# Performance work log

Measured on AMD Instinct MI355X. Metric: run time of the kernel, lower is better.

## Reference

```python
import jax, jax.numpy as jnp
import numpy as np

B, S, TLEN, IN_DI, H = 256, 512, 32, 5, 256  # batch, enc seq len, decode horizon, features, hidden


def setup_inputs() -> dict:
    key = jax.random.key(0)
    ks = jax.random.split(key, 20)
    sc = 0.06  # ~ 1/sqrt(H), matches torch LSTM/Linear uniform init scale
    def p(k, shape):
        return jax.random.normal(k, shape, jnp.float32) * sc
    return {
        "srcs": jax.random.normal(ks[0], (B, S, IN_DI), jnp.float32),
        # encoder LSTM layer 1 (in_di -> H), layer 2 (H -> H); b = b_ih + b_hh combined
        "wih_e1": p(ks[1], (4 * H, IN_DI)), "whh_e1": p(ks[2], (4 * H, H)), "b_e1": p(ks[3], (4 * H,)),
        "wih_e2": p(ks[4], (4 * H, H)), "whh_e2": p(ks[5], (4 * H, H)), "b_e2": p(ks[6], (4 * H,)),
        # decoder input projection Linear(in_di -> H)
        "wdi": p(ks[7], (H, IN_DI)), "bdi": p(ks[8], (H,)),
        # decoder LSTM layer 1 (H -> H), layer 2 (H -> H)
        "wih_d1": p(ks[9], (4 * H, H)), "whh_d1": p(ks[10], (4 * H, H)), "b_d1": p(ks[11], (4 * H,)),
        "wih_d2": p(ks[12], (4 * H, H)), "whh_d2": p(ks[13], (4 * H, H)), "b_d2": p(ks[14], (4 * H,)),
        # w: Linear(2H -> in_di); out_projection: Linear(in_di -> in_di)
        "ww": p(ks[15], (IN_DI, 2 * H)), "bw": p(ks[16], (IN_DI,)),
        "wop": p(ks[17], (IN_DI, IN_DI)), "bop": p(ks[18], (IN_DI,)),
    }


def _cell(h, c, gates_x, whh):
    # pytorch LSTM gate order: i, f, g, o
    g = gates_x + h @ whh.T
    i, f, gg, o = jnp.split(g, 4, axis=-1)
    c = jax.nn.sigmoid(f) * c + jax.nn.sigmoid(i) * jnp.tanh(gg)
    h = jax.nn.sigmoid(o) * jnp.tanh(c)
    return h, c


def _lstm(x, h0, c0, wih, whh, b):
    # x: [B, T, D] -> outs [B, T, H], final (h, c)
    xs = x @ wih.T + b  # precompute input projections [B, T, 4H]
    def step(carry, xt):
        h, c = _cell(carry[0], carry[1], xt, whh)
        return (h, c), h
    (h, c), ys = jax.lax.scan(step, (h0, c0), jnp.swapaxes(xs, 0, 1))
    return jnp.swapaxes(ys, 0, 1), h, c


def reference(srcs, wih_e1, whh_e1, b_e1, wih_e2, whh_e2, b_e2,
              wdi, bdi, wih_d1, whh_d1, b_d1, wih_d2, whh_d2, b_d2,
              ww, bw, wop, bop):
    Bv = srcs.shape[0]
    z = jnp.zeros((Bv, H), srcs.dtype)
    # encoder: two stacked LSTMs, zero initial state (dropout is identity in eval)
    e1, _, _ = _lstm(srcs, z, z, wih_e1, whh_e1, b_e1)
    enc_outs, h_enc, c_enc = _lstm(e1, z, z, wih_e2, whh_e2, b_e2)  # [B, S, H]

    def dec_step(carry, _):
        h, c, inp = carry
        x = inp @ wdi.T + bdi                               # dec_input projection [B, H]
        # decoder LSTM layer 1 seeded with carried hidden (source passes layer-2 hidden back in)
        h1, c1 = _cell(h, c, x @ wih_d1.T + b_d1, whh_d1)
        # decoder LSTM layer 2 re-zeroed every step (faithful to LSTMS_Decoder)
        h2, c2 = _cell(z, z, h1 @ wih_d2.T + b_d2, whh_d2)  # dec_out [B, H]
        energies = jnp.einsum('bh,bsh->bs', h2, enc_outs)   # dot attention
        weights = jax.nn.softmax(energies, axis=0)          # softmax over dim=0 (batch!), as in source
        context = jnp.einsum('bs,bsh->bh', weights, enc_outs)
        cats = jnp.concatenate([h2, context], axis=-1) @ ww.T + bw
        pred = jnp.tanh(cats) @ wop.T + bop                 # [B, in_di]
        return (h2, c2, pred), (pred, context)

    inp0 = jnp.ones((Bv, IN_DI), srcs.dtype)
    _, (preds, ctxs) = jax.lax.scan(dec_step, (h_enc, c_enc, inp0), None, length=TLEN)
    out = jnp.swapaxes(preds, 0, 1)        # [B, tlen, in_di]
    context_enc = jnp.swapaxes(ctxs, 0, 1)  # [B, tlen, H]
    return out, context_enc
```

## Files before the change

### kernel.cpp

```cpp
#include <hip/hip_runtime.h>
#include <hip/hip_bf16.h>

#define B_    256
#define S_    512
#define H_    256
#define TLEN_ 32
#define DI_   5
#define ENCSTRIDE 131072
#define CHUNK 32
#define NCHUNK 16
#define NB 2

__device__ __forceinline__ float bf2f(unsigned short v) {
    return __uint_as_float(((unsigned)v) << 16);
}
__device__ __forceinline__ unsigned short f2bf(float f) {
    __hip_bfloat16 h = __float2bfloat16(f);
    return *reinterpret_cast<unsigned short*>(&h);
}

__global__ __launch_bounds__(256) void init_kernel(float* PRD) {
    int i = blockIdx.x * 256 + threadIdx.x;
    if (i < B_ * DI_) PRD[i] = 1.0f;
}

__global__ __launch_bounds__(256) void packbf_kernel(const float* __restrict__ m,
                                                     ushort4* __restrict__ out) {
    int idx = blockIdx.x * 256 + threadIdx.x;
    int k4 = idx >> 10, n = idx & 1023;
    float4 v = ((const float4*)m)[n * 64 + k4];
    out[idx] = make_ushort4(f2bf(v.x), f2bf(v.y), f2bf(v.z), f2bf(v.w));
}

__global__ __launch_bounds__(256) void weff_kernel(const float* __restrict__ wih_d1,
                                                   const float* __restrict__ wdi,
                                                   const float* __restrict__ bdi,
                                                   const float* __restrict__ b_d1,
                                                   float* __restrict__ weff,
                                                   float* __restrict__ beff) {
    int n = blockIdx.x * 256 + threadIdx.x;
    float acc[DI_] = {0.f, 0.f, 0.f, 0.f, 0.f};
    float accb = 0.f;
    for (int k = 0; k < H_; k++) {
        float w = wih_d1[n * H_ + k];
        accb += w * bdi[k];
#pragma unroll
        for (int m = 0; m < DI_; m++) acc[m] += w * wdi[k * DI_ + m];
    }
#pragma unroll
    for (int m = 0; m < DI_; m++) weff[n * DI_ + m] = acc[m];
    beff[n] = b_d1[n] + accb;
}

__device__ __forceinline__ void dot4(const float4 xv, const float4 w0, const float4 w1,
                                     const float4 w2, const float4 w3,
                                     float& a0, float& a1, float& a2, float& a3) {
    a0 += xv.x * w0.x + xv.y * w0.y + xv.z * w0.z + xv.w * w0.w;
    a1 += xv.x * w1.x + xv.y * w1.y + xv.z * w1.z + xv.w * w1.w;
    a2 += xv.x * w2.x + xv.y * w2.y + xv.z * w2.z + xv.w * w2.w;
    a3 += xv.x * w3.x + xv.y * w3.y + xv.z * w3.z + xv.w * w3.w;
}

__device__ __forceinline__ float4 bf4f(ushort4 u) {
    return make_float4(bf2f(u.x), bf2f(u.y), bf2f(u.z), bf2f(u.w));
}

__device__ __forceinline__ void lstm_epilogue(float a0, float a1, float a2, float a3,
                                              float cold, float& cn, float& hn) {
    float ii = 1.f / (1.f + expf(-a0));
    float ff = 1.f / (1.f + expf(-a1));
    float gg = tanhf(a2);
    float oo = 1.f / (1.f + expf(-a3));
    cn = ff * cold + ii * gg;
    hn = oo * tanhf(cn);
}

__global__ __launch_bounds__(1024) void xproj_kernel(
    const float* __restrict__ h1,
    const ushort4* __restrict__ wpb,
    float* __restrict__ X2)
{
    __shared__ float es[32][260];
    int tid = threadIdx.x, j = tid;
    long r0 = (long)blockIdx.x * 32;

    for (int i = tid; i < 2048; i += 1024) {
        int rr = i >> 6, c4 = i & 63;
        ((float4*)&es[rr][0])[c4] = ((const float4*)(h1 + (r0 + rr) * H_))[c4];
    }
    __syncthreads();

    float acc[32];
#pragma unroll
    for (int r = 0; r < 32; r++) acc[r] = 0.f;
    for (int k4 = 0; k4 < 64; k4++) {
        float4 w = bf4f(wpb[(k4 << 10) + j]);
#pragma unroll
        for (int r = 0; r < 32; r++) {
            float4 h4 = ((const float4*)&es[r][0])[k4];
            acc[r] += h4.x * w.x + h4.y * w.y + h4.z * w.z + h4.w * w.w;
        }
    }
#pragma unroll
    for (int r = 0; r < 32; r++) X2[(r0 + r) * 1024 + j] = acc[r];
}

__global__ __launch_bounds__(1024, 4) void enc_chunk_kernel(
    int ci,
    const float* __restrict__ srcs,
    const float* __restrict__ wih_e1,
    const ushort4* __restrict__ whh_e1p,
    const ushort4* __restrict__ whh_e2p,
    const float* __restrict__ b_e1,
    const float* __restrict__ b_e2,
    const float* __restrict__ X2,
    float* __restrict__ H1G,
    float* __restrict__ C1C,
    float* __restrict__ H2C,
    float* __restrict__ C2C,
    __hip_bfloat16* __restrict__ encbf)
{
    __shared__ float4 red[4][NB][256];
    __shared__ float hb[NB][260];
    __shared__ float sS[NB][160];

    int tid = threadIdx.x;
    int kh = tid >> 8;
    int j  = tid & 255;
    int k40 = kh << 4;

    if (blockIdx.x < 128) {
        if (ci >= NCHUNK) return;
        int b0 = blockIdx.x * NB;
        int ts = ci * CHUNK;

        for (int idx = tid; idx < NB * CHUNK * DI_; idx += 1024) {
            int r = idx / (CHUNK * DI_), off = idx - r * (CHUNK * DI_);
            sS[r][off] = srcs[((long)(b0 + r) * S_ + ts) * DI_ + off];
        }
        float creg = 0.f;
        if (kh < NB) {
            hb[kh][j] = (ci == 0) ? 0.f : H1G[(CHUNK - 1) * 65536 + (b0 + kh) * H_ + j];
            creg = (ci == 0) ? 0.f : C1C[(b0 + kh) * H_ + j];
        }
        float bias0 = b_e1[j], bias1 = b_e1[256 + j], bias2 = b_e1[512 + j], bias3 = b_e1[768 + j];
        float wx[4][DI_];
#pragma unroll
        for (int k = 0; k < DI_; k++) {
            wx[0][k] = wih_e1[j * DI_ + k];
            wx[1][k] = wih_e1[(256 + j) * DI_ + k];
            wx[2][k] = wih_e1[(512 + j) * DI_ + k];
            wx[3][k] = wih_e1[(768 + j) * DI_ + k];
        }

        for (int tt = 0; tt < CHUNK; tt++) {
            __syncthreads();
            float A[NB][4];
#pragma unroll
            for (int bb = 0; bb < NB; bb++) {
                A[bb][0] = 0.f; A[bb][1] = 0.f; A[bb][2] = 0.f; A[bb][3] = 0.f;
            }
            if (kh == 0) {
#pragma unroll
                for (int bb = 0; bb < NB; bb++)
#pragma unroll
                    for (int k = 0; k < DI_; k++) {
                        float xv = sS[bb][tt * DI_ + k];
                        A[bb][0] += xv * wx[0][k];
                        A[bb][1] += xv * wx[1][k];
                        A[bb][2] += xv * wx[2][k];
                        A[bb][3] += xv * wx[3][k];
                    }
            }
#pragma unroll 4
            for (int k4 = k40; k4 < k40 + 16; k4++) {
                float4 w0 = bf4f(whh_e1p[(k4 << 10) + j]);
                float4 w1 = bf4f(whh_e1p[(k4 << 10) + 256 + j]);
                float4 w2 = bf4f(whh_e1p[(k4 << 10) + 512 + j]);
                float4 w3 = bf4f(whh_e1p[(k4 << 10) + 768 + j]);
#pragma unroll
                for (int bb = 0; bb < NB; bb++) {
                    float4 h4 = ((const float4*)&hb[bb][0])[k4];
                    dot4(h4, w0, w1, w2, w3, A[bb][0], A[bb][1], A[bb][2], A[bb][3]);
                }
            }
#pragma unroll
            for (int bb = 0; bb < NB; bb++)
                red[kh][bb][j] = make_float4(A[bb][0], A[bb][1], A[bb][2], A[bb][3]);
            __syncthreads();
            if (kh < NB) {
                float a0 = bias0, a1 = bias1, a2 = bias2, a3 = bias3;
#pragma unroll
                for (int kk = 0; kk < 4; kk++) {
                    float4 v = red[kk][kh][j];
                    a0 += v.x; a1 += v.y; a2 += v.z; a3 += v.w;
                }
                float cn, hn;
                lstm_epilogue(a0, a1, a2, a3, creg, cn, hn);
                creg = cn;
                hb[kh][j] = hn;
                H1G[tt * 65536 + (b0 + kh) * H_ + j] = hn;
            }
        }
        if (kh < NB) C1C[(b0 + kh) * H_ + j] = creg;
    } else {
        if (ci < 1) return;
        int b0 = (blockIdx.x - 128) * NB;
        int us = (ci - 1) * CHUNK;

        float creg = 0.f, hlast = 0.f;
        if (kh < NB) {
            hb[kh][j] = (ci == 1) ? 0.f : H2C[(b0 + kh) * H_ + j];
            creg = (ci == 1) ? 0.f : C2C[(b0 + kh) * H_ + j];
        }
        float bias0 = b_e2[j], bias1 = b_e2[256 + j], bias2 = b_e2[512 + j], bias3 = b_e2[768 + j];

        for (int tt = 0; tt < CHUNK; tt++) {
            __syncthreads();
            float x0 = 0.f, x1 = 0.f, x2 = 0.f, x3 = 0.f;
            if (kh < NB) {
                const float* xrow = X2 + ((long)tt * B_ + b0 + kh) * 1024;
                x0 = xrow[j]; x1 = xrow[256 + j]; x2 = xrow[512 + j]; x3 = xrow[768 + j];
            }
            float A[NB][4];
#pragma unroll
            for (int bb = 0; bb < NB; bb++) {
                A[bb][0] = 0.f; A[bb][1] = 0.f; A[bb][2] = 0.f; A[bb][3] = 0.f;
            }
#pragma unroll 4
            for (int k4 = k40; k4 < k40 + 16; k4++) {
                float4 w0 = bf4f(whh_e2p[(k4 << 10) + j]);
                float4 w1 = bf4f(whh_e2p[(k4 << 10) + 256 + j]);
                float4 w2 = bf4f(whh_e2p[(k4 << 10) + 512 + j]);
                float4 w3 = bf4f(whh_e2p[(k4 << 10) + 768 + j]);
#pragma unroll
                for (int bb = 0; bb < NB; bb++) {
                    float4 h4 = ((const float4*)&hb[bb][0])[k4];
                    dot4(h4, w0, w1, w2, w3, A[bb][0], A[bb][1], A[bb][2], A[bb][3]);
                }
            }
#pragma unroll
            for (int bb = 0; bb < NB; bb++)
                red[kh][bb][j] = make_float4(A[bb][0], A[bb][1], A[bb][2], A[bb][3]);
            __syncthreads();
            if (kh < NB) {
                float a0 = bias0 + x0, a1 = bias1 + x1, a2 = bias2 + x2, a3 = bias3 + x3;
#pragma unroll
                for (int kk = 0; kk < 4; kk++) {
                    float4 v = red[kk][kh][j];
                    a0 += v.x; a1 += v.y; a2 += v.z; a3 += v.w;
                }
                float cn, hn;
                lstm_epilogue(a0, a1, a2, a3, creg, cn, hn);
                creg = cn;
                hlast = hn;
                hb[kh][j] = hn;
                encbf[(long)(b0 + kh) * ENCSTRIDE + (us + tt) * H_ + j] = __float2bfloat16(hn);
            }
        }
        if (kh < NB) {
            H2C[(b0 + kh) * H_ + j] = hlast;
            C2C[(b0 + kh) * H_ + j] = creg;
        }
    }
}

__global__ __launch_bounds__(1024) void dec_step_kernel(
    const float* __restrict__ PRD,
    const float* __restrict__ WEF,
    const float* __restrict__ BEF,
    const ushort4* __restrict__ whhd1p,
    const ushort4* __restrict__ wihd2p,
    const float* __restrict__ b_d2,
    float* __restrict__ H2C,
    float* __restrict__ C2C,
    const __hip_bfloat16* __restrict__ enc,
    float* __restrict__ E)
{
    __shared__ float h2s[260];
    __shared__ float h1s[260];
    __shared__ float h2n[260];
    __shared__ float g[1024];
    __shared__ float prd[8];
    int tid = threadIdx.x;
    int j = tid;
    int b = blockIdx.x;

    if (tid < 256) h2s[tid] = H2C[b * H_ + tid];
    if (tid < DI_) prd[tid] = PRD[b * DI_ + tid];
    __syncthreads();

    {
        float wef[DI_];
#pragma unroll
        for (int m = 0; m < DI_; m++) wef[m] = WEF[j * DI_ + m];
        float a = BEF[j];
#pragma unroll
        for (int m = 0; m < DI_; m++) a += wef[m] * prd[m];
#pragma unroll 4
        for (int k4 = 0; k4 < 64; k4++) {
            float4 w = bf4f(whhd1p[(k4 << 10) + j]);
            float4 h4 = ((const float4*)&h2s[0])[k4];
            a += h4.x * w.x + h4.y * w.y + h4.z * w.z + h4.w * w.w;
        }
        g[j] = a;
    }
    __syncthreads();
    if (tid < 256) {
        int n = tid;
        float cn, hn;
        lstm_epilogue(g[n], g[256 + n], g[512 + n], g[768 + n],
                      C2C[b * H_ + n], cn, hn);
        h1s[n] = hn;
    }
    __syncthreads();

    {
        float a = b_d2[j];
#pragma unroll 4
        for (int k4 = 0; k4 < 64; k4++) {
            float4 w = bf4f(wihd2p[(k4 << 10) + j]);
            float4 h4 = ((const float4*)&h1s[0])[k4];
            a += h4.x * w.x + h4.y * w.y + h4.z * w.z + h4.w * w.w;
        }
        g[j] = a;
    }
    __syncthreads();
    if (tid < 256) {
        int n = tid;
        float cn, hn;
        lstm_epilogue(g[n], g[256 + n], g[512 + n], g[768 + n], 0.f, cn, hn);
        C2C[b * H_ + n] = cn;
        H2C[b * H_ + n] = hn;
        h2n[n] = hn;
    }
    __syncthreads();

    {
        int wv = tid >> 6, lane = tid & 63;
        const __hip_bfloat16* ep = enc + (long)b * ENCSTRIDE;
        float hreg[4];
#pragma unroll
        for (int q = 0; q < 4; q++) hreg[q] = h2n[(lane << 2) + q];
        for (int si = 0; si < 32; si++) {
            int s = wv + (si << 4);
            union { float2 f2; unsigned short u[4]; } uu;
            uu.f2 = *(const float2*)(ep + s * H_ + (lane << 2));
            float p = hreg[0] * bf2f(uu.u[0]) + hreg[1] * bf2f(uu.u[1]) +
                      hreg[2] * bf2f(uu.u[2]) + hreg[3] * bf2f(uu.u[3]);
#pragma unroll
            for (int off = 32; off > 0; off >>= 1) p += __shfl_down(p, off);
            if (lane == 0) E[s * B_ + b] = p;
        }
    }
}

__global__ __launch_bounds__(256) void softmax_kernel(const float* __restrict__ E,
                                                      float* __restrict__ W) {
    __shared__ float red[4];
    int s = blockIdx.x, tid = threadIdx.x;
    float v = E[s * B_ + tid];
    float m = v;
#pragma unroll
    for (int off = 32; off > 0; off >>= 1) m = fmaxf(m, __shfl_down(m, off));
    if ((tid & 63) == 0) red[tid >> 6] = m;
    __syncthreads();
    m = fmaxf(fmaxf(red[0], red[1]), fmaxf(red[2], red[3]));
    __syncthreads();
    float e = expf(v - m);
    float p = e;
#pragma unroll
    for (int off = 32; off > 0; off >>= 1) p += __shfl_down(p, off);
    if ((tid & 63) == 0) red[tid >> 6] = p;
    __syncthreads();
    float sum = red[0] + red[1] + red[2] + red[3];
    W[s * B_ + tid] = e / sum;
}

__global__ __launch_bounds__(256) void ctx_out_kernel(
    const float* __restrict__ W,
    const __hip_bfloat16* __restrict__ enc,
    const float* __restrict__ h2,
    const float* __restrict__ ww, const float* __restrict__ bw,
    const float* __restrict__ wop, const float* __restrict__ bop,
    float* __restrict__ out_ctx,
    float* __restrict__ out0,
    float* __restrict__ pred)
{
    __shared__ float lw[S_];
    __shared__ float hc[512];
    int b = blockIdx.x, tid = threadIdx.x;
    lw[tid] = W[tid * B_ + b];
    lw[256 + tid] = W[(256 + tid) * B_ + b];
    hc[tid] = h2[b * H_ + tid];
    __syncthreads();
    float acc = 0.f;
    const __hip_bfloat16* ep = enc + (long)b * ENCSTRIDE + tid;
#pragma unroll 8
    for (int s = 0; s < S_; s++) acc += lw[s] * __bfloat162float(ep[s * H_]);
    out_ctx[(long)b * (TLEN_ * H_) + tid] = acc;
    hc[256 + tid] = acc;
    __syncthreads();
    if (tid < 64) {
        float a[DI_] = {0.f, 0.f, 0.f, 0.f, 0.f};
        for (int k = tid; k < 2 * H_; k += 64) {
            float v = hc[k];
#pragma unroll
            for (int m = 0; m < DI_; m++) a[m] += v * ww[m * (2 * H_) + k];
        }
#pragma unroll
        for (int m = 0; m < DI_; m++)
            for (int off = 32; off > 0; off >>= 1) a[m] += __shfl_down(a[m], off);
        if (tid == 0) {
            float t5[DI_];
#pragma unroll
            for (int m = 0; m < DI_; m++) t5[m] = tanhf(a[m] + bw[m]);
#pragma unroll
            for (int m2 = 0; m2 < DI_; m2++) {
                float o = bop[m2];
#pragma unroll
                for (int m = 0; m < DI_; m++) o += t5[m] * wop[m2 * DI_ + m];
                out0[(long)b * (TLEN_ * DI_) + m2] = o;
                pred[b * DI_ + m2] = o;
            }
        }
    }
}

extern "C" void kernel_launch(void* const* d_in, const int* in_sizes, int n_in,
                              void* d_out, int out_size, void* d_ws, size_t ws_size,
                              hipStream_t stream) {
    const float* srcs   = (const float*)d_in[0];
    const float* wih_e1 = (const float*)d_in[1];
    const float* whh_e1 = (const float*)d_in[2];
    const float* b_e1   = (const float*)d_in[3];
    const float* wih_e2 = (const float*)d_in[4];
    const float* whh_e2 = (const float*)d_in[5];
    const float* b_e2   = (const float*)d_in[6];
    const float* wdi    = (const float*)d_in[7];
    const float* bdi    = (const float*)d_in[8];
    const float* wih_d1 = (const float*)d_in[9];
    const float* whh_d1 = (const float*)d_in[10];
    const float* b_d1   = (const float*)d_in[11];
    const float* wih_d2 = (const float*)d_in[12];
    const float* whh_d2 = (const float*)d_in[13];
    const float* b_d2   = (const float*)d_in[14];
    const float* ww     = (const float*)d_in[15];
    const float* bw     = (const float*)d_in[16];
    const float* wop    = (const float*)d_in[17];
    const float* bop    = (const float*)d_in[18];

    float* ws = (float*)d_ws;
    __hip_bfloat16* ENCBF = (__hip_bfloat16*)d_ws;
    size_t o = 16777216;
    ushort4* PKE1B = (ushort4*)(ws + o); o += 131072;
    ushort4* PKH2B = (ushort4*)(ws + o); o += 131072;
    ushort4* PKD1B = (ushort4*)(ws + o); o += 131072;
    ushort4* PKD2B = (ushort4*)(ws + o); o += 131072;
    ushort4* PKX2B = (ushort4*)(ws + o); o += 131072;
    float* H1G = ws + o; o += 2097152;
    float* X2G = ws + o; o += 8388608;
    float* C1C = ws + o; o += 65536;
    float* H2C = ws + o; o += 65536;
    float* C2C = ws + o; o += 65536;
    float* EN  = ws + o; o += 131072;
    float* WSM = ws + o; o += 131072;
    float* PRD = ws + o; o += 1280;
    float* WEF = ws + o; o += 5120;
    float* BEF = ws + o; o += 1024;

    float* OUT0 = (float*)d_out;
    float* OUT1 = OUT0 + (size_t)B_ * TLEN_ * DI_;

    dim3 t256(256);

    init_kernel<<<dim3(8), t256, 0, stream>>>(PRD);

    packbf_kernel<<<dim3(256), t256, 0, stream>>>(whh_e1, PKE1B);
    packbf_kernel<<<dim3(256), t256, 0, stream>>>(whh_e2, PKH2B);
    packbf_kernel<<<dim3(256), t256, 0, stream>>>(whh_d1, PKD1B);
    packbf_kernel<<<dim3(256), t256, 0, stream>>>(wih_d2, PKD2B);
    packbf_kernel<<<dim3(256), t256, 0, stream>>>(wih_e2, PKX2B);
    weff_kernel<<<dim3(4), t256, 0, stream>>>(wih_d1, wdi, bdi, b_d1, WEF, BEF);

    for (int ci = 0; ci <= NCHUNK; ci++) {
        enc_chunk_kernel<<<dim3(256), dim3(1024), 0, stream>>>(
            ci, srcs, wih_e1, PKE1B, PKH2B, b_e1, b_e2,
            X2G, H1G, C1C, H2C, C2C, ENCBF);
        if (ci < NCHUNK) {
            xproj_kernel<<<dim3(256), dim3(1024), 0, stream>>>(H1G, PKX2B, X2G);
        }
    }

    for (int t = 0; t < TLEN_; t++) {
        dec_step_kernel<<<dim3(256), dim3(1024), 0, stream>>>(
            PRD, WEF, BEF, PKD1B, PKD2B, b_d2, H2C, C2C, ENCBF, EN);
        softmax_kernel<<<dim3(512), t256, 0, stream>>>(EN, WSM);
        ctx_out_kernel<<<dim3(256), t256, 0, stream>>>(
            WSM, ENCBF, H2C, ww, bw, wop, bop,
            OUT1 + (size_t)t * H_, OUT0 + (size_t)t * DI_, PRD);
    }
}
```

Measured before the change: 8.363 ms.

## Fuse context/output with next decoder LSTM step and energy computation

```diff
diff --git a/kernel.cpp b/kernel.cpp
--- a/kernel.cpp
+++ b/kernel.cpp
@@ -377,30 +377,57 @@
     W[s * B_ + tid] = e / sum;
 }
 
-__global__ __launch_bounds__(256) void ctx_out_kernel(
+__global__ __launch_bounds__(1024) void dec_fused_kernel(
+    int t,
     const float* __restrict__ W,
     const __hip_bfloat16* __restrict__ enc,
-    const float* __restrict__ h2,
+    float* __restrict__ H2C,
+    float* __restrict__ C2C,
+    const float* __restrict__ WEF,
+    const float* __restrict__ BEF,
+    const ushort4* __restrict__ whhd1p,
+    const ushort4* __restrict__ wihd2p,
+    const float* __restrict__ b_d2,
     const float* __restrict__ ww, const float* __restrict__ bw,
     const float* __restrict__ wop, const float* __restrict__ bop,
     float* __restrict__ out_ctx,
     float* __restrict__ out0,
-    float* __restrict__ pred)
+    float* __restrict__ E)
 {
-    __shared__ float lw[S_];
+    __shared__ float lw[512];
+    __shared__ float h2s[260];
+    __shared__ float pc[4][256];
     __shared__ float hc[512];
-    int b = blockIdx.x, tid = threadIdx.x;
-    lw[tid] = W[tid * B_ + b];
-    lw[256 + tid] = W[(256 + tid) * B_ + b];
-    hc[tid] = h2[b * H_ + tid];
-    __syncthreads();
-    float acc = 0.f;
-    const __hip_bfloat16* ep = enc + (long)b * ENCSTRIDE + tid;
+    __shared__ float prd[8];
+    __shared__ float h1s[260];
+    __shared__ float h2n[260];
+    __shared__ float g[1024];
+    int tid = threadIdx.x;
+    int j = tid;
+    int b = blockIdx.x;
+
+    if (tid < 512) lw[tid] = W[tid * B_ + b];
+    else if (tid < 768) h2s[tid - 512] = H2C[b * H_ + (tid - 512)];
+    __syncthreads();
+
+    {
+        int sh = tid >> 8, jj = tid & 255;
+        const __hip_bfloat16* ep = enc + (long)b * ENCSTRIDE + jj;
+        float acc = 0.f;
+        int s0 = sh << 7;
 #pragma unroll 8
-    for (int s = 0; s < S_; s++) acc += lw[s] * __bfloat162float(ep[s * H_]);
-    out_ctx[(long)b * (TLEN_ * H_) + tid] = acc;
-    hc[256 + tid] = acc;
-    __syncthreads();
+        for (int s = s0; s < s0 + 128; s++) acc += lw[s] * __bfloat162float(ep[s * H_]);
+        pc[sh][jj] = acc;
+    }
+    __syncthreads();
+    if (tid < 256) {
+        float cx = pc[0][tid] + pc[1][tid] + pc[2][tid] + pc[3][tid];
+        out_ctx[(long)b * (TLEN_ * H_) + tid] = cx;
+        hc[tid] = h2s[tid];
+        hc[256 + tid] = cx;
+    }
+    __syncthreads();
+
     if (tid < 64) {
         float a[DI_] = {0.f, 0.f, 0.f, 0.f, 0.f};
         for (int k = tid; k < 2 * H_; k += 64) {
@@ -421,8 +448,74 @@
 #pragma unroll
                 for (int m = 0; m < DI_; m++) o += t5[m] * wop[m2 * DI_ + m];
                 out0[(long)b * (TLEN_ * DI_) + m2] = o;
-                pred[b * DI_ + m2] = o;
-            }
+                prd[m2] = o;
+            }
+        }
+    }
+    if (t == TLEN_ - 1) return;
+    __syncthreads();
+
+    {
+        float wef[DI_];
+#pragma unroll
+        for (int m = 0; m < DI_; m++) wef[m] = WEF[j * DI_ + m];
+        float a = BEF[j];
+#pragma unroll
+        for (int m = 0; m < DI_; m++) a += wef[m] * prd[m];
+#pragma unroll 4
+        for (int k4 = 0; k4 < 64; k4++) {
+            float4 w = bf4f(whhd1p[(k4 << 10) + j]);
+            float4 h4 = ((const float4*)&h2s[0])[k4];
+            a += h4.x * w.x + h4.y * w.y + h4.z * w.z + h4.w * w.w;
+        }
+        g[j] = a;
+    }
+    __syncthreads();
+    if (tid < 256) {
+        int n = tid;
+        float cn, hn;
+        lstm_epilogue(g[n], g[256 + n], g[512 + n], g[768 + n],
+                      C2C[b * H_ + n], cn, hn);
+        h1s[n] = hn;
+    }
+    __syncthreads();
+
+    {
+        float a = b_d2[j];
+#pragma unroll 4
+        for (int k4 = 0; k4 < 64; k4++) {
+            float4 w = bf4f(wihd2p[(k4 << 10) + j]);
+            float4 h4 = ((const float4*)&h1s[0])[k4];
+            a += h4.x * w.x + h4.y * w.y + h4.z * w.z + h4.w * w.w;
+        }
+        g[j] = a;
+    }
+    __syncthreads();
+    if (tid < 256) {
+        int n = tid;
+        float cn, hn;
+        lstm_epilogue(g[n], g[256 + n], g[512 + n], g[768 + n], 0.f, cn, hn);
+        C2C[b * H_ + n] = cn;
+        H2C[b * H_ + n] = hn;
+        h2n[n] = hn;
+    }
+    __syncthreads();
+
+    {
+        int wv = tid >> 6, lane = tid & 63;
+        const __hip_bfloat16* ep = enc + (long)b * ENCSTRIDE;
+        float hreg[4];
+#pragma unroll
+        for (int q = 0; q < 4; q++) hreg[q] = h2n[(lane << 2) + q];
+        for (int si = 0; si < 32; si++) {
+            int s = wv + (si << 4);
+            union { float2 f2; unsigned short u[4]; } uu;
+            uu.f2 = *(const float2*)(ep + s * H_ + (lane << 2));
+            float p = hreg[0] * bf2f(uu.u[0]) + hreg[1] * bf2f(uu.u[1]) +
+                      hreg[2] * bf2f(uu.u[2]) + hreg[3] * bf2f(uu.u[3]);
+#pragma unroll
+            for (int off = 32; off > 0; off >>= 1) p += __shfl_down(p, off);
+            if (lane == 0) E[s * B_ + b] = p;
         }
     }
 }
@@ -492,12 +585,13 @@
         }
     }
 
+    dec_step_kernel<<<dim3(256), dim3(1024), 0, stream>>>(
+        PRD, WEF, BEF, PKD1B, PKD2B, b_d2, H2C, C2C, ENCBF, EN);
     for (int t = 0; t < TLEN_; t++) {
-        dec_step_kernel<<<dim3(256), dim3(1024), 0, stream>>>(
-            PRD, WEF, BEF, PKD1B, PKD2B, b_d2, H2C, C2C, ENCBF, EN);
         softmax_kernel<<<dim3(512), t256, 0, stream>>>(EN, WSM);
-        ctx_out_kernel<<<dim3(256), t256, 0, stream>>>(
-            WSM, ENCBF, H2C, ww, bw, wop, bop,
-            OUT1 + (size_t)t * H_, OUT0 + (size_t)t * DI_, PRD);
-    }
-}
+        dec_fused_kernel<<<dim3(256), dim3(1024), 0, stream>>>(
+            t, WSM, ENCBF, H2C, C2C, WEF, BEF, PKD1B, PKD2B, b_d2,
+            ww, bw, wop, bop,
+            OUT1 + (size_t)t * H_, OUT0 + (size_t)t * DI_, EN);
+    }
+}
```

Measured after the change: 7.925 ms, median of 2. -5.2%, faster.
